# Performance work log

Measured on AMD Instinct MI355X. Metric: run time of the kernel, lower is better.

The kernel has to match this reference:

```python
import jax, jax.numpy as jnp
import numpy as np

D_MODEL = 512
NUM_HEADS = 8
HEAD_DIM = D_MODEL // NUM_HEADS  # 64
EMBEDDING_DIM = 512  # undefined global EmbeddingDim in source -> d_model
EVENT_DIM = 388      # undefined global EventDim in source -> MIDI event vocab
B, T = 2, 2048


def setup_inputs() -> dict:
    key = jax.random.key(0)
    ks = jax.random.split(key, 12)
    sc = 0.02
    v = jax.random.normal(ks[0], (B, T, D_MODEL), jnp.float32)
    k = jax.random.normal(ks[1], (B, T, D_MODEL), jnp.float32)
    q = jax.random.normal(ks[2], (B, T, D_MODEL), jnp.float32)
    mask = jnp.tril(jnp.ones((T, T), jnp.float32))  # causal mask, broadcasts to [H,B,T,T]
    Wq = jax.random.normal(ks[3], (D_MODEL, HEAD_DIM), jnp.float32) * sc
    bq = jnp.zeros((HEAD_DIM,), jnp.float32)
    Wk = jax.random.normal(ks[4], (D_MODEL, HEAD_DIM), jnp.float32) * sc
    bk = jnp.zeros((HEAD_DIM,), jnp.float32)
    Wv = jax.random.normal(ks[5], (D_MODEL, HEAD_DIM), jnp.float32) * sc
    bv = jnp.zeros((HEAD_DIM,), jnp.float32)
    E = jax.random.normal(ks[6], (NUM_HEADS, T, HEAD_DIM), jnp.float32) * sc
    Wo = jax.random.normal(ks[7], (D_MODEL, EMBEDDING_DIM), jnp.float32) * sc
    bo = jnp.zeros((EMBEDDING_DIM,), jnp.float32)
    Wl = jax.random.normal(ks[8], (EMBEDDING_DIM, EVENT_DIM), jnp.float32) * sc
    bl = jnp.zeros((EVENT_DIM,), jnp.float32)
    return {"v": v, "k": k, "q": q, "mask": mask, "Wq": Wq, "bq": bq,
            "Wk": Wk, "bk": bk, "Wv": Wv, "bv": bv, "E": E,
            "Wo": Wo, "bo": bo, "Wl": Wl, "bl": bl}


def _skew(S):
    # S: [H,B,T,T] -> Music-Transformer skew via left-pad, reshape, slice
    H, Bb, Tt, _ = S.shape
    S = jnp.pad(S, ((0, 0), (0, 0), (0, 0), (1, 0)))          # [H,B,T,T+1]
    S = S.reshape(H, Bb, Tt + 1, Tt)                           # [H,B,T+1,T]
    return S[:, :, 1:]                                         # [H,B,T,T]


def reference(v, k, q, mask, Wq, bq, Wk, bk, Wv, bv, E, Wo, bo, Wl, bl):
    # The source applies the SAME Dense per head, so all heads share q/k/v projections
    qh = q @ Wq + bq  # [B,T,hd]
    kh = k @ Wk + bk  # [B,T,hd]
    vh = v @ Wv + bv  # [B,T,hd]
    # relative-position scores per head: Q @ E^T then skew
    S = jnp.einsum('btd,hsd->hbts', qh, E)  # [H,B,T,T]
    S = _skew(S)
    qk = jnp.einsum('btd,bsd->bts', qh, kh)  # [B,T,T], identical across heads
    attn = (qk[None] + S) / np.sqrt(HEAD_DIM)  # [H,B,T,T]
    attn = attn * mask - jnp.asarray(1e10, attn.dtype) * (1.0 - mask)
    score = jax.nn.softmax(attn, axis=-1)
    ctx = jnp.einsum('hbts,bsd->hbtd', score, vh)  # [H,B,T,hd]
    ctx = jnp.transpose(ctx, (1, 2, 0, 3)).reshape(ctx.shape[1], ctx.shape[2], -1)  # [B,T,d_model]
    ctx = jax.nn.relu(ctx @ Wo + bo)  # [B,T,EmbeddingDim]
    logits = ctx @ Wl + bl            # [B,T,EventDim]
    return logits
```

## Files before the change

### kernel.cpp

```cpp
#include <hip/hip_runtime.h>
#include <hip/hip_bf16.h>


#define B_ 2
#define T_ 2048
#define DM_ 512
#define H_ 8
#define HD_ 64
#define ED_ 512
#define EV_ 388
#define BT_ (B_ * T_)

typedef __attribute__((ext_vector_type(8))) short short8;
typedef __attribute__((ext_vector_type(4))) float floatx4;

#define MFMA(a, b, c) __builtin_amdgcn_mfma_f32_16x16x32_bf16((a), (b), (c), 0, 0, 0)

__device__ __forceinline__ float bfs(unsigned short s) {
  union { unsigned int i; float f; } v; v.i = ((unsigned int)s) << 16; return v.f;
}
__device__ __forceinline__ unsigned short f2bf(float f) {
  __hip_bfloat16 h = __float2bfloat16(f);
  union { __hip_bfloat16 h; unsigned short u; } v; v.h = h; return v.u;
}
__device__ __forceinline__ float ldf(const void* p, int i, bool isbf) {
  return isbf ? bfs(((const unsigned short*)p)[i]) : ((const float*)p)[i];
}
__device__ __forceinline__ bool det_bf(const unsigned int* mask) {
  return mask[0] != 0x3F800000u;
}
__device__ __forceinline__ void gl_lds16(const unsigned short* g, void* l) {
  __builtin_amdgcn_global_load_lds(
      (const __attribute__((address_space(1))) void*)g,
      (__attribute__((address_space(3))) void*)l, 16, 0, 0);
}

__global__ __launch_bounds__(256) void prep_kernel(
    const void* __restrict__ E, const void* __restrict__ Wq,
    const void* __restrict__ Wk, const void* __restrict__ Wv,
    const void* __restrict__ Wo, const void* __restrict__ Wl,
    const unsigned int* __restrict__ mask,
    unsigned short* __restrict__ E_c, unsigned short* __restrict__ WqT,
    unsigned short* __restrict__ WkT, unsigned short* __restrict__ WvT,
    unsigned short* __restrict__ WoT, unsigned short* __restrict__ WlT) {
  const bool isbf = det_bf(mask);
  const int tid = threadIdx.x;
  int bi = blockIdx.x;
  if (bi < 1024) {
    const int i0 = (bi * 256 + tid) * 4;
    if (isbf) {
      *(uint2*)&E_c[i0] = *(const uint2*)((const unsigned short*)E + i0);
    } else {
      float4 f = *(const float4*)((const float*)E + i0);
      unsigned short p[4] = {f2bf(f.x), f2bf(f.y), f2bf(f.z), f2bf(f.w)};
      *(uint2*)&E_c[i0] = *(uint2*)p;
    }
    return;
  }
  bi -= 1024;
  const void* src; unsigned short* dst; int N, nb;
  if (bi < 16)       { src = Wq; dst = WqT; N = 64;  nb = bi; }
  else if (bi < 32)  { src = Wk; dst = WkT; N = 64;  nb = bi - 16; }
  else if (bi < 48)  { src = Wv; dst = WvT; N = 64;  nb = bi - 32; }
  else if (bi < 176) { src = Wo; dst = WoT; N = 512; nb = bi - 48; }
  else               { src = Wl; dst = WlT; N = 388; nb = bi - 176; }
  const int n = nb * 4 + (tid >> 6);
  const int k0 = (tid & 63) * 8;
  unsigned short vv[8];
#pragma unroll
  for (int j = 0; j < 8; ++j) {
    if (n >= N) vv[j] = 0;
    else if (isbf) vv[j] = ((const unsigned short*)src)[(size_t)(k0 + j) * N + n];
    else vv[j] = f2bf(((const float*)src)[(size_t)(k0 + j) * N + n]);
  }
  *(uint4*)&dst[(size_t)n * DM_ + k0] = *(uint4*)vv;
}

__global__ __launch_bounds__(256) void gemm_proj(
    const void* __restrict__ xq, const void* __restrict__ xk,
    const void* __restrict__ xv,
    const unsigned short* __restrict__ WqT, const unsigned short* __restrict__ WkT,
    const unsigned short* __restrict__ WvT,
    const void* __restrict__ bq, const void* __restrict__ bk,
    const void* __restrict__ bv, const unsigned int* __restrict__ mask,
    unsigned short* __restrict__ oq, unsigned short* __restrict__ ok,
    unsigned short* __restrict__ ovt) {
  __shared__ __align__(16) short sA[64][72];
  __shared__ __align__(16) short sW[64][72];
  const int sel = blockIdx.y;
  const void* x = (sel == 0) ? xq : (sel == 1) ? xk : xv;
  const unsigned short* WT = (sel == 0) ? WqT : (sel == 1) ? WkT : WvT;
  const void* bias = (sel == 0) ? bq : (sel == 1) ? bk : bv;
  const bool isbf = det_bf(mask);

  const int tid = threadIdx.x;
  const int w = tid >> 6, lane = tid & 63;
  const int q_ = lane >> 4, n_ = lane & 15;
  const int row0 = blockIdx.x * 64;

  floatx4 acc[4];
#pragma unroll
  for (int j = 0; j < 4; ++j) acc[j] = (floatx4){0.f, 0.f, 0.f, 0.f};

  for (int k0 = 0; k0 < DM_; k0 += 64) {
    if (isbf) {
#pragma unroll
      for (int it = 0; it < 2; ++it) {
        int idx = tid + it * 256;
        int rr = idx >> 3, cc = (idx & 7) * 8;
        *(uint4*)&sA[rr][cc] =
            *(const uint4*)((const unsigned short*)x + (size_t)(row0 + rr) * DM_ + k0 + cc);
      }
    } else {
#pragma unroll
      for (int it = 0; it < 4; ++it) {
        int idx = tid + it * 256;
        int rr = idx >> 4, cc = (idx & 15) * 4;
        float4 f = *(const float4*)((const float*)x + (size_t)(row0 + rr) * DM_ + k0 + cc);
        unsigned short p[4] = {f2bf(f.x), f2bf(f.y), f2bf(f.z), f2bf(f.w)};
        *(uint2*)&sA[rr][cc] = *(uint2*)p;
      }
    }
#pragma unroll
    for (int it = 0; it < 2; ++it) {
      int idx = tid + it * 256;
      int rr = idx >> 3, cc = (idx & 7) * 8;
      *(uint4*)&sW[rr][cc] = *(const uint4*)(WT + (size_t)rr * DM_ + k0 + cc);
    }
    __syncthreads();
    short8 a0 = *(const short8*)&sA[16 * w + n_][8 * q_];
    short8 a1 = *(const short8*)&sA[16 * w + n_][32 + 8 * q_];
#pragma unroll
    for (int nb = 0; nb < 4; ++nb) {
      short8 b0 = *(const short8*)&sW[16 * nb + n_][8 * q_];
      short8 b1 = *(const short8*)&sW[16 * nb + n_][32 + 8 * q_];
      acc[nb] = MFMA(a0, b0, acc[nb]);
      acc[nb] = MFMA(a1, b1, acc[nb]);
    }
    __syncthreads();
  }

#pragma unroll
  for (int nb = 0; nb < 4; ++nb) {
    const int col = 16 * nb + n_;
    const float bb = ldf(bias, col, isbf);
#pragma unroll
    for (int r = 0; r < 4; ++r) {
      int row = row0 + 16 * w + 4 * q_ + r;
      unsigned short val = f2bf(acc[nb][r] + bb);
      if (sel < 2) {
        unsigned short* o = (sel == 0) ? oq : ok;
        o[(size_t)row * HD_ + col] = val;
      } else {
        int b = row >> 11, s = row & 2047;
        ovt[(((size_t)(b * HD_ + col)) << 11) + s] = val;
      }
    }
  }
}

__device__ __forceinline__ int pbase_of(int ti) {
  return (ti < 22) ? (ti - 11) * 2 : 22 + (ti - 22) * 3;
}

__global__ __launch_bounds__(256, 4) void attn_kernel(
    const unsigned short* __restrict__ qh, const unsigned short* __restrict__ kh,
    const unsigned short* __restrict__ vt, const unsigned short* __restrict__ E,
    unsigned short* __restrict__ ctxo, float* __restrict__ pc,
    float* __restrict__ ml) {
  __shared__ __align__(16) short sK[2][64][64];
  __shared__ __align__(16) short sVT[2][64][64];
  __shared__ __align__(16) short sP[64][64];

  const int id = blockIdx.x;
  const int hb = id & 15;
  const int rem = id >> 4;
  int ti, c, nc;
  if (rem < 11)      { ti = rem;                  c = 0;              nc = 1; }
  else if (rem < 33) { ti = 11 + ((rem - 11) >> 1); c = (rem - 11) & 1; nc = 2; }
  else               { ti = 22 + (rem - 33) / 3;    c = (rem - 33) % 3; nc = 3; }
  const int nsteps = ti + 1;
  const int klo = (c * nsteps) / nc;
  const int khi = ((c + 1) * nsteps) / nc;

  const int h = hb >> 1, b = hb & 1;
  const int t0 = ti * 64;

  const int tid = threadIdx.x;
  const int w = tid >> 6, lane = tid & 63;
  const int q_ = lane >> 4, n_ = lane & 15;

  const int trow = t0 + 16 * w + n_;
  const unsigned short* qp = qh + (((size_t)((b << 11) + trow)) << 6) + (q_ << 3);
  const short8 qa0 = *(const short8*)qp;
  const short8 qa1 = *(const short8*)(qp + 32);

  short8 onesf;
#pragma unroll
  for (int j = 0; j < 8; ++j) onesf[j] = (short)0x3F80;

  floatx4 ctxa[4];
#pragma unroll
  for (int nb = 0; nb < 4; ++nb) ctxa[nb] = (floatx4){0.f, 0.f, 0.f, 0.f};
  floatx4 lacc = (floatx4){0.f, 0.f, 0.f, 0.f};

  const unsigned short* eb = E + ((size_t)h << 17);
  const unsigned short* kbase = kh + (((size_t)(b << 11)) << 6);
  const unsigned short* vbase = vt + (((size_t)(b << 6)) << 11);

  const int lrow = lane >> 3;
  const int lchunk = ((lane & 7) ^ lrow) << 3;
  const int rK0 = 8 * w + lrow;
  const int c0s = ((q_ ^ (n_ & 7)) << 3);
  const int c1s = (((q_ | 4) ^ (n_ & 7)) << 3);

#define STAGE(bufsel, s0v)                                                     \
  {                                                                            \
    void* dK = (void*)&sK[bufsel][8 * w][0];                                   \
    void* dV = (void*)&sVT[bufsel][8 * w][0];                                  \
    const unsigned short* gK =                                                 \
        kbase + (((size_t)((s0v) + rK0)) << 6) + lchunk;                       \
    const unsigned short* gV =                                                 \
        vbase + (((size_t)rK0) << 11) + (s0v) + lchunk;                        \
    gl_lds16(gK, dK);                                                          \
    gl_lds16(gK + (32 << 6), (void*)((short*)dK + 32 * 64));                   \
    gl_lds16(gV, dV);                                                          \
    gl_lds16(gV + (32 << 11), (void*)((short*)dV + 32 * 64));                  \
  }

#define ELOAD(s0v)                                                             \
  {                                                                            \
    const int rb_ = (T_ - 64) + (s0v)-t0;                                      \
    _Pragma("unroll") for (int f = 0; f < 5; ++f) {                            \
      int gr = rb_ + 16 * (3 - w + f) + n_;                                    \
      if (gr > T_ - 1) gr = T_ - 1;           \
      const unsigned short* ep = eb + ((size_t)gr << 6) + (q_ << 3);           \
      e0[f] = *(const short8*)ep;                                              \
      e1[f] = *(const short8*)(ep + 32);                                       \
    }                                                                          \
  }

  short8 e0[5], e1[5];
  STAGE(0, klo * 64);
  ELOAD(klo * 64);

  for (int kt = klo; kt < khi; ++kt) {
    const int cur = (kt - klo) & 1;
    const int s0 = kt * 64;

    asm volatile("s_waitcnt vmcnt(0)" ::: "memory");
    __builtin_amdgcn_sched_barrier(0);
    __builtin_amdgcn_s_barrier();
    __builtin_amdgcn_sched_barrier(0);

    if (kt + 1 < khi) STAGE(cur ^ 1, s0 + 64);

    floatx4 qk[4];
    __builtin_amdgcn_s_setprio(1);
#pragma unroll
    for (int nb = 0; nb < 4; ++nb) {
      short8 kb0 = *(const short8*)&sK[cur][16 * nb + n_][c0s];
      short8 kb1 = *(const short8*)&sK[cur][16 * nb + n_][c1s];
      qk[nb] = (floatx4){0.f, 0.f, 0.f, 0.f};
      qk[nb] = MFMA(qa0, kb0, qk[nb]);
      qk[nb] = MFMA(qa1, kb1, qk[nb]);
    }
    floatx4 qe[5];
#pragma unroll
    for (int f = 0; f < 5; ++f) {
      qe[f] = (floatx4){0.f, 0.f, 0.f, 0.f};
      qe[f] = MFMA(qa0, e0[f], qe[f]);
      qe[f] = MFMA(qa1, e1[f], qe[f]);
    }
    __builtin_amdgcn_s_setprio(0);

    if (kt + 1 < khi) ELOAD(s0 + 64);

    const bool diag = (kt == ti);
#pragma unroll
    for (int r = 0; r < 4; ++r) {
      const int t = 4 * q_ + r;
      const int ba = ((q_ << 4) | ((n_ - t + 15) & 15)) << 2;
      const int nd = (n_ + t + 1) & 15;
      const bool hi = nd > t;
      const int swr = (t & 7) << 3;
#pragma unroll
      for (int mb = 0; mb < 4; ++mb) {
        float merged = hi ? qe[mb + 1][r] : qe[mb][r];
        float g = __int_as_float(
            __builtin_amdgcn_ds_bpermute(ba, __float_as_int(merged)));
        float sv = qk[mb][r] + g;
        if (diag && (16 * mb + n_ > 16 * w + t)) sv = -1.0e30f;
        sP[16 * w + t][(16 * mb + n_) ^ swr] =
            (short)f2bf(exp2f(sv * 0.18033688011f));
      }
    }

    short8 pa0 = *(const short8*)&sP[16 * w + n_][c0s];
    short8 pa1 = *(const short8*)&sP[16 * w + n_][c1s];
    __builtin_amdgcn_s_setprio(1);
#pragma unroll
    for (int nb = 0; nb < 4; ++nb) {
      short8 v0 = *(const short8*)&sVT[cur][16 * nb + n_][c0s];
      short8 v1 = *(const short8*)&sVT[cur][16 * nb + n_][c1s];
      ctxa[nb] = MFMA(pa0, v0, ctxa[nb]);
      ctxa[nb] = MFMA(pa1, v1, ctxa[nb]);
    }
    lacc = MFMA(pa0, onesf, lacc);
    lacc = MFMA(pa1, onesf, lacc);
    __builtin_amdgcn_s_setprio(0);
  }
#undef STAGE
#undef ELOAD

  if (nc == 1) {
#pragma unroll
    for (int r = 0; r < 4; ++r) {
      const float inv = 1.0f / lacc[r];
      const int row = t0 + 16 * w + 4 * q_ + r;
      const size_t base = (((size_t)((b << 11) + row)) << 9) + (h << 6) + n_;
#pragma unroll
      for (int nb = 0; nb < 4; ++nb)
        ctxo[base + 16 * nb] = f2bf(ctxa[nb][r] * inv);
    }
  } else {
    const int idx = hb * 52 + pbase_of(ti) + c;
    float* pcb = pc + ((size_t)idx << 12);
    float* mlb = ml + ((size_t)idx << 6);
#pragma unroll
    for (int r = 0; r < 4; ++r) {
      const int row = 16 * w + 4 * q_ + r;
#pragma unroll
      for (int nb = 0; nb < 4; ++nb)
        pcb[(row << 6) + 16 * nb + n_] = ctxa[nb][r];
      if (n_ == 0) mlb[row] = lacc[r];
    }
  }
}

__global__ __launch_bounds__(256) void combine_kernel(
    const float* __restrict__ pc, const float* __restrict__ ml,
    unsigned short* __restrict__ ctxo) {
  const int cb = blockIdx.x;
  const int hb = cb / 21;
  const int ti = 11 + cb % 21;
  const int nc = (ti < 22) ? 2 : 3;
  const int h = hb >> 1, b = hb & 1, t0 = ti * 64;
  const int tid = threadIdx.x;
  const int row = tid >> 2, seg = (tid & 3) * 16;
  const int idx0 = hb * 52 + pbase_of(ti);

  float lsum = 0.f;
  float4 a4[4];
#pragma unroll
  for (int j = 0; j < 4; ++j) a4[j] = (float4){0.f, 0.f, 0.f, 0.f};
  for (int c = 0; c < nc; ++c) {
    const int idx = idx0 + c;
    lsum += ml[((size_t)idx << 6) + row];
    const float* cp = pc + ((size_t)idx << 12) + (row << 6) + seg;
#pragma unroll
    for (int j = 0; j < 4; ++j) {
      float4 x = *(const float4*)(cp + 4 * j);
      a4[j].x += x.x; a4[j].y += x.y; a4[j].z += x.z; a4[j].w += x.w;
    }
  }
  const float inv = 1.0f / lsum;
  unsigned short o[16];
#pragma unroll
  for (int j = 0; j < 4; ++j) {
    o[4 * j + 0] = f2bf(a4[j].x * inv);
    o[4 * j + 1] = f2bf(a4[j].y * inv);
    o[4 * j + 2] = f2bf(a4[j].z * inv);
    o[4 * j + 3] = f2bf(a4[j].w * inv);
  }
  unsigned short* dst =
      ctxo + (((size_t)((b << 11) + t0 + row)) << 9) + (h << 6) + seg;
  *(uint4*)dst = *(uint4*)&o[0];
  *(uint4*)(dst + 8) = *(uint4*)&o[8];
}

template <int RELU>
__global__ __launch_bounds__(256) void mlp_mfma(
    const unsigned short* __restrict__ A, const unsigned short* __restrict__ WT,
    const void* __restrict__ bias, unsigned short* __restrict__ outBF,
    void* __restrict__ outD, const unsigned int* __restrict__ mask) {
  __shared__ __align__(16) short sA[64][72];
  __shared__ __align__(16) short sW[64][72];
  const int tid = threadIdx.x;
  const int w = tid >> 6, lane = tid & 63;
  const int q_ = lane >> 4, n_ = lane & 15;
  const int row0 = blockIdx.x * 64;
  const int n0 = blockIdx.y * 64;
  const bool isbf = det_bf(mask);

  floatx4 acc[4];
#pragma unroll
  for (int j = 0; j < 4; ++j) acc[j] = (floatx4){0.f, 0.f, 0.f, 0.f};

  for (int k0 = 0; k0 < DM_; k0 += 64) {
#pragma unroll
    for (int it = 0; it < 2; ++it) {
      int idx = tid + it * 256;
      int rr = idx >> 3, cc = (idx & 7) * 8;
      *(uint4*)&sA[rr][cc] = *(const uint4*)(A + (size_t)(row0 + rr) * DM_ + k0 + cc);
      *(uint4*)&sW[rr][cc] = *(const uint4*)(WT + (size_t)(n0 + rr) * DM_ + k0 + cc);
    }
    __syncthreads();
    short8 a0 = *(const short8*)&sA[16 * w + n_][8 * q_];
    short8 a1 = *(const short8*)&sA[16 * w + n_][32 + 8 * q_];
#pragma unroll
    for (int nb = 0; nb < 4; ++nb) {
      short8 b0 = *(const short8*)&sW[16 * nb + n_][8 * q_];
      short8 b1 = *(const short8*)&sW[16 * nb + n_][32 + 8 * q_];
      acc[nb] = MFMA(a0, b0, acc[nb]);
      acc[nb] = MFMA(a1, b1, acc[nb]);
    }
    __syncthreads();
  }

#pragma unroll
  for (int nb = 0; nb < 4; ++nb) {
    const int col = n0 + 16 * nb + n_;
    float bb = 0.f;
    if (RELU || col < EV_) bb = ldf(bias, col, isbf);
#pragma unroll
    for (int r = 0; r < 4; ++r) {
      const int row = row0 + 16 * w + 4 * q_ + r;
      float v = acc[nb][r] + bb;
      if (RELU) {
        outBF[(size_t)row * ED_ + col] = f2bf(fmaxf(v, 0.f));
      } else if (col < EV_) {
        if (isbf) ((unsigned short*)outD)[(size_t)row * EV_ + col] = f2bf(v);
        else      ((float*)outD)[(size_t)row * EV_ + col] = v;
      }
    }
  }
}

extern "C" void kernel_launch(void* const* d_in, const int* in_sizes, int n_in,
                              void* d_out, int out_size, void* d_ws, size_t ws_size,
                              hipStream_t stream) {
  const void* v  = d_in[0];
  const void* k  = d_in[1];
  const void* q  = d_in[2];
  const unsigned int* mask = (const unsigned int*)d_in[3];
  const void* Wq = d_in[4];
  const void* bq = d_in[5];
  const void* Wk = d_in[6];
  const void* bk = d_in[7];
  const void* Wv = d_in[8];
  const void* bv = d_in[9];
  const void* E  = d_in[10];
  const void* Wo = d_in[11];
  const void* bo = d_in[12];
  const void* Wl = d_in[13];
  const void* bl = d_in[14];

  char* p = (char*)d_ws;
  unsigned short* E_c  = (unsigned short*)p; p += (size_t)H_ * T_ * HD_ * 2;
  unsigned short* qhb  = (unsigned short*)p; p += (size_t)BT_ * HD_ * 2;
  unsigned short* khb  = (unsigned short*)p; p += (size_t)BT_ * HD_ * 2;
  unsigned short* vtb  = (unsigned short*)p; p += (size_t)BT_ * HD_ * 2;
  unsigned short* WqT  = (unsigned short*)p; p += (size_t)HD_ * DM_ * 2;
  unsigned short* WkT  = (unsigned short*)p; p += (size_t)HD_ * DM_ * 2;
  unsigned short* WvT  = (unsigned short*)p; p += (size_t)HD_ * DM_ * 2;
  unsigned short* WoT  = (unsigned short*)p; p += (size_t)ED_ * DM_ * 2;
  unsigned short* WlT  = (unsigned short*)p; p += (size_t)448 * DM_ * 2;
  unsigned short* ctxb = (unsigned short*)p; p += (size_t)BT_ * DM_ * 2;
  unsigned short* h1b  = (unsigned short*)p; p += (size_t)BT_ * ED_ * 2;
  float* pc = (float*)p; p += (size_t)16 * 52 * 4096 * 4;
  float* ml = (float*)p; p += (size_t)16 * 52 * 64 * 4;

  prep_kernel<<<dim3(1312), 256, 0, stream>>>(
      E, Wq, Wk, Wv, Wo, Wl, mask, E_c, WqT, WkT, WvT, WoT, WlT);
  gemm_proj<<<dim3(BT_ / 64, 3), 256, 0, stream>>>(
      q, k, v, WqT, WkT, WvT, bq, bk, bv, mask, qhb, khb, vtb);
  attn_kernel<<<dim3(1008), 256, 0, stream>>>(qhb, khb, vtb, E_c, ctxb, pc, ml);
  combine_kernel<<<dim3(336), 256, 0, stream>>>(pc, ml, ctxb);
  mlp_mfma<1><<<dim3(BT_ / 64, ED_ / 64), 256, 0, stream>>>(
      ctxb, WoT, bo, h1b, nullptr, mask);
  mlp_mfma<0><<<dim3(BT_ / 64, 448 / 64), 256, 0, stream>>>(
      h1b, WlT, bl, nullptr, d_out, mask);
}
```

Measured before the change: 231.1 us.

## Stage relative-position E tiles through LDS and rebalance split-K attention schedule

```diff
diff --git a/kernel.cpp b/kernel.cpp
--- a/kernel.cpp
+++ b/kernel.cpp
@@ -160,25 +160,28 @@
 }
 
 __device__ __forceinline__ int pbase_of(int ti) {
-  return (ti < 22) ? (ti - 11) * 2 : 22 + (ti - 22) * 3;
-}
-
-__global__ __launch_bounds__(256, 4) void attn_kernel(
+  return (ti < 16) ? (ti - 8) * 2 : (ti < 24) ? 16 + (ti - 16) * 3
+                                              : 40 + (ti - 24) * 4;
+}
+
+__global__ __launch_bounds__(256, 2) void attn_kernel(
     const unsigned short* __restrict__ qh, const unsigned short* __restrict__ kh,
     const unsigned short* __restrict__ vt, const unsigned short* __restrict__ E,
     unsigned short* __restrict__ ctxo, float* __restrict__ pc,
     float* __restrict__ ml) {
   __shared__ __align__(16) short sK[2][64][64];
   __shared__ __align__(16) short sVT[2][64][64];
+  __shared__ __align__(16) short sE[2][128][64];
   __shared__ __align__(16) short sP[64][64];
 
   const int id = blockIdx.x;
   const int hb = id & 15;
-  const int rem = id >> 4;
+  const int rem = 79 - (id >> 4);
   int ti, c, nc;
-  if (rem < 11)      { ti = rem;                  c = 0;              nc = 1; }
-  else if (rem < 33) { ti = 11 + ((rem - 11) >> 1); c = (rem - 11) & 1; nc = 2; }
-  else               { ti = 22 + (rem - 33) / 3;    c = (rem - 33) % 3; nc = 3; }
+  if (rem < 8)       { ti = rem;                 c = 0;            nc = 1; }
+  else if (rem < 24) { ti = 8 + ((rem - 8) >> 1);  c = (rem - 8) & 1;  nc = 2; }
+  else if (rem < 48) { ti = 16 + (rem - 24) / 3;   c = (rem - 24) % 3; nc = 3; }
+  else               { ti = 24 + ((rem - 48) >> 2); c = (rem - 48) & 3; nc = 4; }
   const int nsteps = ti + 1;
   const int klo = (c * nsteps) / nc;
   const int khi = ((c + 1) * nsteps) / nc;
@@ -208,41 +211,32 @@
   const unsigned short* kbase = kh + (((size_t)(b << 11)) << 6);
   const unsigned short* vbase = vt + (((size_t)(b << 6)) << 11);
 
-  const int lrow = lane >> 3;
-  const int lchunk = ((lane & 7) ^ lrow) << 3;
-  const int rK0 = 8 * w + lrow;
+  const int lrow8 = lane >> 3;
+  const int lch = ((lane & 7) ^ lrow8) << 3;
+  const int rK0 = 8 * w + lrow8;
   const int c0s = ((q_ ^ (n_ & 7)) << 3);
   const int c1s = (((q_ | 4) ^ (n_ & 7)) << 3);
 
 #define STAGE(bufsel, s0v)                                                     \
   {                                                                            \
-    void* dK = (void*)&sK[bufsel][8 * w][0];                                   \
-    void* dV = (void*)&sVT[bufsel][8 * w][0];                                  \
     const unsigned short* gK =                                                 \
-        kbase + (((size_t)((s0v) + rK0)) << 6) + lchunk;                       \
+        kbase + (((size_t)((s0v) + rK0)) << 6) + lch;                          \
     const unsigned short* gV =                                                 \
-        vbase + (((size_t)rK0) << 11) + (s0v) + lchunk;                        \
-    gl_lds16(gK, dK);                                                          \
-    gl_lds16(gK + (32 << 6), (void*)((short*)dK + 32 * 64));                   \
-    gl_lds16(gV, dV);                                                          \
-    gl_lds16(gV + (32 << 11), (void*)((short*)dV + 32 * 64));                  \
-  }
-
-#define ELOAD(s0v)                                                             \
-  {                                                                            \
-    const int rb_ = (T_ - 64) + (s0v)-t0;                                      \
-    _Pragma("unroll") for (int f = 0; f < 5; ++f) {                            \
-      int gr = rb_ + 16 * (3 - w + f) + n_;                                    \
+        vbase + (((size_t)rK0) << 11) + (s0v) + lch;                           \
+    gl_lds16(gK, (void*)&sK[bufsel][8 * w][0]);                                \
+    gl_lds16(gK + (32 << 6), (void*)(&sK[bufsel][8 * w][0] + 32 * 64));        \
+    gl_lds16(gV, (void*)&sVT[bufsel][8 * w][0]);                               \
+    gl_lds16(gV + (32 << 11), (void*)(&sVT[bufsel][8 * w][0] + 32 * 64));      \
+    const int rbE = (T_ - 64) + (s0v)-t0;                                      \
+    _Pragma("unroll") for (int off = 0; off < 4; ++off) {                      \
+      int gr = rbE + 32 * w + 8 * off + lrow8;                                 \
       if (gr > T_ - 1) gr = T_ - 1;           \
-      const unsigned short* ep = eb + ((size_t)gr << 6) + (q_ << 3);           \
-      e0[f] = *(const short8*)ep;                                              \
-      e1[f] = *(const short8*)(ep + 32);                                       \
+      gl_lds16(eb + ((size_t)gr << 6) + lch,                                   \
+               (void*)&sE[bufsel][32 * w + 8 * off][0]);                       \
     }                                                                          \
   }
 
-  short8 e0[5], e1[5];
   STAGE(0, klo * 64);
-  ELOAD(klo * 64);
 
   for (int kt = klo; kt < khi; ++kt) {
     const int cur = (kt - klo) & 1;
@@ -268,13 +262,14 @@
     floatx4 qe[5];
 #pragma unroll
     for (int f = 0; f < 5; ++f) {
+      const short* ep = &sE[cur][16 * (3 - w + f) + n_][0];
+      short8 eb0 = *(const short8*)(ep + c0s);
+      short8 eb1 = *(const short8*)(ep + c1s);
       qe[f] = (floatx4){0.f, 0.f, 0.f, 0.f};
-      qe[f] = MFMA(qa0, e0[f], qe[f]);
-      qe[f] = MFMA(qa1, e1[f], qe[f]);
+      qe[f] = MFMA(qa0, eb0, qe[f]);
+      qe[f] = MFMA(qa1, eb1, qe[f]);
     }
     __builtin_amdgcn_s_setprio(0);
-
-    if (kt + 1 < khi) ELOAD(s0 + 64);
 
     const bool diag = (kt == ti);
 #pragma unroll
@@ -311,7 +306,6 @@
     __builtin_amdgcn_s_setprio(0);
   }
 #undef STAGE
-#undef ELOAD
 
   if (nc == 1) {
 #pragma unroll
@@ -324,7 +318,7 @@
         ctxo[base + 16 * nb] = f2bf(ctxa[nb][r] * inv);
     }
   } else {
-    const int idx = hb * 52 + pbase_of(ti) + c;
+    const int idx = hb * 72 + pbase_of(ti) + c;
     float* pcb = pc + ((size_t)idx << 12);
     float* mlb = ml + ((size_t)idx << 6);
 #pragma unroll
@@ -342,13 +336,13 @@
     const float* __restrict__ pc, const float* __restrict__ ml,
     unsigned short* __restrict__ ctxo) {
   const int cb = blockIdx.x;
-  const int hb = cb / 21;
-  const int ti = 11 + cb % 21;
-  const int nc = (ti < 22) ? 2 : 3;
+  const int hb = cb / 24;
+  const int ti = 8 + cb % 24;
+  const int nc = (ti >> 3) + 1;
   const int h = hb >> 1, b = hb & 1, t0 = ti * 64;
   const int tid = threadIdx.x;
   const int row = tid >> 2, seg = (tid & 3) * 16;
-  const int idx0 = hb * 52 + pbase_of(ti);
+  const int idx0 = hb * 72 + pbase_of(ti);
 
   float lsum = 0.f;
   float4 a4[4];
@@ -468,15 +462,15 @@
   unsigned short* WlT  = (unsigned short*)p; p += (size_t)448 * DM_ * 2;
   unsigned short* ctxb = (unsigned short*)p; p += (size_t)BT_ * DM_ * 2;
   unsigned short* h1b  = (unsigned short*)p; p += (size_t)BT_ * ED_ * 2;
-  float* pc = (float*)p; p += (size_t)16 * 52 * 4096 * 4;
-  float* ml = (float*)p; p += (size_t)16 * 52 * 64 * 4;
+  float* pc = (float*)p; p += (size_t)16 * 72 * 4096 * 4;
+  float* ml = (float*)p; p += (size_t)16 * 72 * 64 * 4;
 
   prep_kernel<<<dim3(1312), 256, 0, stream>>>(
       E, Wq, Wk, Wv, Wo, Wl, mask, E_c, WqT, WkT, WvT, WoT, WlT);
   gemm_proj<<<dim3(BT_ / 64, 3), 256, 0, stream>>>(
       q, k, v, WqT, WkT, WvT, bq, bk, bv, mask, qhb, khb, vtb);
-  attn_kernel<<<dim3(1008), 256, 0, stream>>>(qhb, khb, vtb, E_c, ctxb, pc, ml);
-  combine_kernel<<<dim3(336), 256, 0, stream>>>(pc, ml, ctxb);
+  attn_kernel<<<dim3(1280), 256, 0, stream>>>(qhb, khb, vtb, E_c, ctxb, pc, ml);
+  combine_kernel<<<dim3(384), 256, 0, stream>>>(pc, ml, ctxb);
   mlp_mfma<1><<<dim3(BT_ / 64, ED_ / 64), 256, 0, stream>>>(
       ctxb, WoT, bo, h1b, nullptr, mask);
   mlp_mfma<0><<<dim3(BT_ / 64, 448 / 64), 256, 0, stream>>>(
```

Result: faster. 202.5 us (-12.4%).
